# Performance work log

Measured on AMD Instinct MI355X. Metric: run time of the kernel, lower is better.

The kernel has to match this reference:

```python
import jax, jax.numpy as jnp
import numpy as np

EPS = 1e-06


def _conv1x1(x, W, b):
    # x: [B,C,H,W], W: [O,C], b: [O] -> [B,O,H,W]
    return jnp.einsum('oc,bchw->bohw', W, x) + b[None, :, None, None]


def _l2_norm(x):
    # normalize over channel dim (-2) per position, matching torch.norm(p=2, dim=-2)
    return x / jnp.linalg.norm(x, axis=-2, keepdims=True)


def setup_inputs() -> dict:
    key = jax.random.key(0)
    ks = jax.random.split(key, 8)
    B, C, H, W = 8, 512, 64, 64
    Cq = C // 8
    s = 0.02
    return {
        'x': jax.random.normal(ks[0], (B, C, H, W), jnp.float32),
        'Wq': jax.random.normal(ks[1], (Cq, C), jnp.float32) * s,
        'bq': jax.random.normal(ks[2], (Cq,), jnp.float32) * s,
        'Wk': jax.random.normal(ks[3], (Cq, C), jnp.float32) * s,
        'bk': jax.random.normal(ks[4], (Cq,), jnp.float32) * s,
        'Wv': jax.random.normal(ks[5], (C, C), jnp.float32) * s,
        'bv': jax.random.normal(ks[6], (C,), jnp.float32) * s,
        'gamma': jax.random.normal(ks[7], (1,), jnp.float32),
    }


def reference(x, Wq, bq, Wk, bk, Wv, bv, gamma):
    B, C, H, W = x.shape
    N = H * W
    Q = _conv1x1(x, Wq, bq).reshape(B, -1, N)   # [B,C',N]
    K = _conv1x1(x, Wk, bk).reshape(B, -1, N)   # [B,C',N]
    V = _conv1x1(x, Wv, bv).reshape(B, C, N)    # [B,C,N]

    Qn = _l2_norm(Q).transpose(0, 2, 1)         # [B,N,C']
    Kn = _l2_norm(K)                            # [B,C',N]

    # taylor denominator: 1 / (N + Q . (sum_n K + eps))
    tailor_sum = 1.0 / (N + jnp.einsum('bnc,bc->bn', Qn, Kn.sum(-1) + EPS))  # [B,N]

    value_sum = V.sum(-1)                        # [B,C]
    matrix = jnp.einsum('bmn,bcn->bmc', Kn, V)   # [B,C',C]
    matrix_sum = value_sum[:, :, None] + jnp.einsum('bnm,bmc->bcn', Qn, matrix)  # [B,C,N]

    weight_value = (matrix_sum * tailor_sum[:, None, :]).reshape(B, C, H, W)
    return gamma * weight_value
```

## Files before the change

### kernel.cpp

```cpp
#include <hip/hip_runtime.h>
#include <math.h>

#define B_   8
#define C_   512
#define CQ   64
#define N_   4096
#define EPSF 1e-6f
#define LS   40
#define LS2  72
#define LSF  552

typedef short  shortx8 __attribute__((ext_vector_type(8)));
typedef short  shortx4 __attribute__((ext_vector_type(4)));
typedef short  shortx2 __attribute__((ext_vector_type(2)));
typedef float  floatx4 __attribute__((ext_vector_type(4)));
typedef float  floatx2 __attribute__((ext_vector_type(2)));

__device__ __forceinline__ short f2bf(float f) {
    unsigned u = __builtin_bit_cast(unsigned, f);
    u += 0x7FFFu + ((u >> 16) & 1u);
    return (short)(u >> 16);
}
__device__ __forceinline__ float bf2f(short h) {
    unsigned u = ((unsigned)(unsigned short)h) << 16;
    return __builtin_bit_cast(float, u);
}
__device__ __forceinline__ shortx8 ldf8(const short* p) {
    return *(const shortx8*)p;
}

__global__ __launch_bounds__(256) void pcast(
    const float* __restrict__ Wq, const float* __restrict__ Wk,
    const float* __restrict__ Wv, short* __restrict__ Wqk, short* __restrict__ Wvb)
{
    int i = (blockIdx.x * 256 + threadIdx.x) * 4;
    float4 v; short* dst;
    if (i < 2 * CQ * C_) {
        const float* src = (i < CQ * C_) ? (Wq + i) : (Wk + i - CQ * C_);
        v = *(const float4*)src;
        dst = Wqk + i;
    } else {
        int j = i - 2 * CQ * C_;
        v = *(const float4*)(Wv + j);
        dst = Wvb + j;
    }
    const float* f = (const float*)&v;
    shortx4 o = { f2bf(f[0]), f2bf(f[1]), f2bf(f[2]), f2bf(f[3]) };
    *(shortx4*)dst = o;
}

__global__ __launch_bounds__(256, 2) void k1_qk(
    const float* __restrict__ x, const short* __restrict__ Wqk,
    const float* __restrict__ bq, const float* __restrict__ bk,
    short* __restrict__ Qnt, short* __restrict__ Kn, float* __restrict__ Ksum)
{
    const int b   = blockIdx.y;
    const int n0  = blockIdx.x * 64;
    const int tid = threadIdx.x;
    const int lane = tid & 63, wid = tid >> 6;
    const int waveM = wid >> 1, waveN = wid & 1;
    const int quad = lane >> 4, ln = lane & 15;

    __shared__ __attribute__((aligned(16))) short B_l[64][LSF];
    __shared__ float bias_l[128];

    if (tid < 128) bias_l[tid] = (tid < 64) ? bq[tid] : bk[tid - 64];

    const int nq = tid & 15, kp = tid >> 4;
    const float* xb = x + (size_t)b * C_ * N_;
#pragma unroll 4
    for (int i = 0; i < 16; i++) {
        const int k = kp * 2 + 32 * i;
        const float* p = xb + (size_t)k * N_ + n0 + nq * 4;
        float4 r0 = *(const float4*)(p);
        float4 r1 = *(const float4*)(p + N_);
        const float* f0 = (const float*)&r0;
        const float* f1 = (const float*)&r1;
#pragma unroll
        for (int j = 0; j < 4; j++) {
            shortx2 t = { f2bf(f0[j]), f2bf(f1[j]) };
            *(shortx2*)&B_l[nq * 4 + j][k] = t;
        }
    }
    __syncthreads();

    const short* Ab = Wqk + (size_t)(waveM * 64 + ln) * C_ + quad * 8;
    const floatx4 z4 = {0.f, 0.f, 0.f, 0.f};
    floatx4 acc[4][2];
#pragma unroll
    for (int mt = 0; mt < 4; mt++) { acc[mt][0] = z4; acc[mt][1] = z4; }

#pragma unroll 4
    for (int kc = 0; kc < 16; ++kc) {
        shortx8 af[4];
#pragma unroll
        for (int mt = 0; mt < 4; mt++)
            af[mt] = ldf8(Ab + (size_t)mt * 16 * C_ + kc * 32);
#pragma unroll
        for (int nt = 0; nt < 2; nt++) {
            shortx8 bf8 = ldf8(&B_l[waveN * 32 + nt * 16 + ln][kc * 32 + quad * 8]);
#pragma unroll
            for (int mt = 0; mt < 4; mt++)
                acc[mt][nt] = __builtin_amdgcn_mfma_f32_16x16x32_bf16(af[mt], bf8, acc[mt][nt], 0, 0, 0);
        }
    }

#pragma unroll
    for (int mt = 0; mt < 4; mt++)
#pragma unroll
        for (int r = 0; r < 4; r++) {
            float bias = bias_l[waveM * 64 + mt * 16 + quad * 4 + r];
#pragma unroll
            for (int nt = 0; nt < 2; nt++) acc[mt][nt][r] += bias;
        }
#pragma unroll
    for (int nt = 0; nt < 2; nt++) {
        float s = 0.f;
#pragma unroll
        for (int mt = 0; mt < 4; mt++)
#pragma unroll
            for (int r = 0; r < 4; r++) s += acc[mt][nt][r] * acc[mt][nt][r];
        s += __shfl_xor(s, 16);
        s += __shfl_xor(s, 32);
        float inv = rsqrtf(s);
#pragma unroll
        for (int mt = 0; mt < 4; mt++)
#pragma unroll
            for (int r = 0; r < 4; r++) acc[mt][nt][r] *= inv;
    }

    if (waveM == 0) {
        short* Qb = Qnt + (size_t)b * N_ * CQ;
#pragma unroll
        for (int nt = 0; nt < 2; nt++) {
            int n = n0 + waveN * 32 + nt * 16 + ln;
#pragma unroll
            for (int mt = 0; mt < 4; mt++) {
                shortx4 v;
#pragma unroll
                for (int r = 0; r < 4; r++) v[r] = f2bf(acc[mt][nt][r]);
                *(shortx4*)(Qb + (size_t)n * CQ + mt * 16 + quad * 4) = v;
            }
        }
    } else {
        short* Kb = Kn + (size_t)b * CQ * N_;
#pragma unroll
        for (int mt = 0; mt < 4; mt++)
#pragma unroll
            for (int r = 0; r < 4; r++) {
                int m = mt * 16 + quad * 4 + r;
                float s = 0.f;
#pragma unroll
                for (int nt = 0; nt < 2; nt++) {
                    int n = n0 + waveN * 32 + nt * 16 + ln;
                    float v = acc[mt][nt][r];
                    Kb[(size_t)m * N_ + n] = f2bf(v);
                    s += v;
                }
                s += __shfl_xor(s, 1); s += __shfl_xor(s, 2);
                s += __shfl_xor(s, 4); s += __shfl_xor(s, 8);
                if (ln == 0) atomicAdd(&Ksum[b * CQ + m], s);
            }
    }
}

__global__ __launch_bounds__(256, 2) void k2_kx(
    const float* __restrict__ x, const short* __restrict__ Kn,
    float* __restrict__ KX, float* __restrict__ xsum)
{
    const int jt = blockIdx.x, ks = blockIdx.y, b = blockIdx.z;
    const int j0 = jt * 64, nbase = ks * 512;
    const int tid = threadIdx.x;
    const int lane = tid & 63, wid = tid >> 6;
    const int quad = lane >> 4, ln = lane & 15;

    __shared__ __attribute__((aligned(16))) short B_l[64][LSF];

    const int rA = tid >> 2, oA = (tid & 3) * 8;
    const float* xb = x + (size_t)b * C_ * N_;
    const float* Bs = xb + (size_t)(j0 + rA) * N_ + nbase;

    float xsacc = 0.f;
#pragma unroll 4
    for (int i = 0; i < 16; i++) {
        const int n = oA + 32 * i;
        float4 b0 = *(const float4*)(Bs + n);
        float4 b1 = *(const float4*)(Bs + n + 4);
        const float* f0 = (const float*)&b0;
        const float* f1 = (const float*)&b1;
        shortx8 t;
#pragma unroll
        for (int q = 0; q < 4; q++) {
            t[q]     = f2bf(f0[q]); xsacc += f0[q];
            t[q + 4] = f2bf(f1[q]); xsacc += f1[q];
        }
        *(shortx8*)&B_l[rA][n] = t;
    }
    __syncthreads();

    const short* Kb = Kn + (size_t)b * CQ * N_;
    const short* Ab = Kb + (size_t)ln * N_ + nbase + quad * 8;
    const floatx4 z4 = {0.f, 0.f, 0.f, 0.f};
    floatx4 acc[4] = {z4, z4, z4, z4};

#pragma unroll 4
    for (int kc = 0; kc < 16; ++kc) {
        shortx8 af[4];
#pragma unroll
        for (int mt = 0; mt < 4; mt++)
            af[mt] = ldf8(Ab + (size_t)mt * 16 * N_ + kc * 32);
        shortx8 bf8 = ldf8(&B_l[wid * 16 + ln][kc * 32 + quad * 8]);
#pragma unroll
        for (int mt = 0; mt < 4; mt++)
            acc[mt] = __builtin_amdgcn_mfma_f32_16x16x32_bf16(af[mt], bf8, acc[mt], 0, 0, 0);
    }

    xsacc += __shfl_xor(xsacc, 1);
    xsacc += __shfl_xor(xsacc, 2);
    if ((tid & 3) == 0) atomicAdd(&xsum[b * C_ + j0 + rA], xsacc);

    float* KXb = KX + (size_t)b * CQ * C_;
#pragma unroll
    for (int mt = 0; mt < 4; mt++)
#pragma unroll
        for (int r = 0; r < 4; r++) {
            int m = mt * 16 + quad * 4 + r;
            atomicAdd(&KXb[(size_t)m * C_ + j0 + wid * 16 + ln], acc[mt][r]);
        }
}

__global__ __launch_bounds__(256, 2) void k3_m(
    const float* __restrict__ KX, const short* __restrict__ Wvb,
    const float* __restrict__ bv, const float* __restrict__ Ksum,
    const float* __restrict__ xsum,
    short* __restrict__ Mt, float* __restrict__ vs)
{
    const int ct = blockIdx.x, b = blockIdx.y;
    const int c0 = ct * 64;
    const int tid = threadIdx.x;
    const int lane = tid & 63, wid = tid >> 6;
    const int quad = lane >> 4, ln = lane & 15;

    __shared__ short A_l[2][64][LS];
    __shared__ short B_l[2][64][LS];
    __shared__ float xsl[C_], Ksl[64], bvl[64], vsp[4][64];

    xsl[tid] = xsum[(size_t)b * C_ + tid];
    xsl[tid + 256] = xsum[(size_t)b * C_ + tid + 256];
    if (tid < 64) { Ksl[tid] = Ksum[b * CQ + tid]; bvl[tid] = bv[c0 + tid]; }

    const int rA = tid >> 2, oA = (tid & 3) * 8;
    const short* As = Wvb + (size_t)(c0 + rA) * C_ + oA;
    const float* Bs = KX + ((size_t)b * CQ + rA) * C_ + oA;

    shortx8 aC = *(const shortx8*)As;
    float4 b0 = *(const float4*)(Bs);
    float4 b1 = *(const float4*)(Bs + 4);

    auto stage = [&](int buf, shortx8 a, float4 q0, float4 q1) {
        *(shortx8*)&A_l[buf][rA][oA] = a;
        const float* f0 = (const float*)&q0;
        const float* f1 = (const float*)&q1;
        shortx8 t;
#pragma unroll
        for (int i = 0; i < 4; i++) { t[i] = f2bf(f0[i]); t[i + 4] = f2bf(f1[i]); }
        *(shortx8*)&B_l[buf][rA][oA] = t;
    };
    stage(0, aC, b0, b1);
    __syncthreads();

    const floatx4 z4 = {0.f, 0.f, 0.f, 0.f};
    floatx4 acc[4] = {z4, z4, z4, z4};
    float vsacc = 0.f;
    const int cv = tid & 63;

    int cur = 0;
    for (int it = 0; it < 16; ++it) {
        shortx8 aN; float4 n0v, n1v;
        if (it < 15) {
            const int off = (it + 1) * 32;
            aN  = *(const shortx8*)(As + off);
            n0v = *(const float4*)(Bs + off);
            n1v = *(const float4*)(Bs + off + 4);
        }
        shortx8 af[4];
#pragma unroll
        for (int ct2 = 0; ct2 < 4; ct2++)
            af[ct2] = ldf8(&A_l[cur][ct2 * 16 + ln][quad * 8]);
        shortx8 bf8 = ldf8(&B_l[cur][wid * 16 + ln][quad * 8]);
#pragma unroll
        for (int ct2 = 0; ct2 < 4; ct2++)
            acc[ct2] = __builtin_amdgcn_mfma_f32_16x16x32_bf16(af[ct2], bf8, acc[ct2], 0, 0, 0);
#pragma unroll
        for (int jj = 0; jj < 8; jj++)
            vsacc += bf2f(A_l[cur][cv][wid * 8 + jj]) * xsl[it * 32 + wid * 8 + jj];
        if (it < 15) stage(cur ^ 1, aN, n0v, n1v);
        __syncthreads();
        cur ^= 1;
    }

    vsp[wid][cv] = vsacc;
    __syncthreads();
    if (tid < 64)
        vs[(size_t)b * C_ + c0 + tid] =
            vsp[0][tid] + vsp[1][tid] + vsp[2][tid] + vsp[3][tid] + (float)N_ * bvl[tid];

    const int m = wid * 16 + ln;
    const float ksm = Ksl[m];
    short* Mb = Mt + (size_t)b * C_ * CQ;
#pragma unroll
    for (int ct2 = 0; ct2 < 4; ct2++)
#pragma unroll
        for (int r = 0; r < 4; r++) {
            int c = ct2 * 16 + quad * 4 + r;
            Mb[(size_t)(c0 + c) * CQ + m] = f2bf(acc[ct2][r] + ksm * bvl[c]);
        }
}

__global__ __launch_bounds__(256, 3) void k4_out(
    const short* __restrict__ Qnt, const short* __restrict__ Mt,
    const float* __restrict__ vs, const float* __restrict__ Ksum,
    const float* __restrict__ gamma, float* __restrict__ out)
{
    const int nt = blockIdx.x, ct = blockIdx.y, b = blockIdx.z;
    const int n0 = nt * 128, c0 = ct * 128;
    const int tid = threadIdx.x;
    const int lane = tid & 63, wid = tid >> 6;
    const int waveC = wid >> 1, waveN = wid & 1;
    const int quad = lane >> 4, ln = lane & 15;

    __shared__ short A_l[128][LS2];
    __shared__ short B_l[128][LS2];
    __shared__ float tsl[128], vsl[128], Ks_l[64];

    {
        int c = tid >> 1, h = tid & 1;
        const short* src = Mt + ((size_t)b * C_ + c0 + c) * CQ + h * 32;
#pragma unroll
        for (int q = 0; q < 4; q++)
            *(shortx8*)&A_l[c][h * 32 + q * 8] = *(const shortx8*)(src + q * 8);
    }
    {
        int n = tid >> 1, h = tid & 1;
        const short* src = Qnt + ((size_t)b * N_ + n0 + n) * CQ + h * 32;
#pragma unroll
        for (int q = 0; q < 4; q++)
            *(shortx8*)&B_l[n][h * 32 + q * 8] = *(const shortx8*)(src + q * 8);
    }
    if (tid < 64)  Ks_l[tid] = Ksum[b * CQ + tid];
    if (tid < 128) vsl[tid]  = vs[(size_t)b * C_ + c0 + tid];
    __syncthreads();

    if (tid < 128) {
        const short* row = B_l[tid];
        float s = 0.f;
#pragma unroll
        for (int m = 0; m < 64; m++) s += bf2f(row[m]) * (Ks_l[m] + EPSF);
        tsl[tid] = 1.f / ((float)N_ + s);
    }
    __syncthreads();

    const floatx4 z4 = {0.f, 0.f, 0.f, 0.f};
    floatx4 acc[4][4];
#pragma unroll
    for (int i = 0; i < 4; i++)
#pragma unroll
        for (int j = 0; j < 4; j++) acc[i][j] = z4;

#pragma unroll
    for (int kc = 0; kc < 2; kc++) {
        shortx8 af[4];
#pragma unroll
        for (int ct2 = 0; ct2 < 4; ct2++)
            af[ct2] = ldf8(&A_l[waveC * 64 + ct2 * 16 + ln][kc * 32 + quad * 8]);
#pragma unroll
        for (int nt2 = 0; nt2 < 4; nt2++) {
            shortx8 bf8 = ldf8(&B_l[waveN * 64 + nt2 * 16 + ln][kc * 32 + quad * 8]);
#pragma unroll
            for (int ct2 = 0; ct2 < 4; ct2++)
                acc[ct2][nt2] = __builtin_amdgcn_mfma_f32_16x16x32_bf16(af[ct2], bf8, acc[ct2][nt2], 0, 0, 0);
        }
    }

    const float g = gamma[0];
    float* ob = out + (size_t)b * C_ * N_;
#pragma unroll
    for (int ct2 = 0; ct2 < 4; ct2++)
#pragma unroll
        for (int r = 0; r < 4; r++) {
            int cl = waveC * 64 + ct2 * 16 + quad * 4 + r;
            float vc = vsl[cl];
#pragma unroll
            for (int nt2 = 0; nt2 < 4; nt2++) {
                int nl = waveN * 64 + nt2 * 16 + ln;
                ob[(size_t)(c0 + cl) * N_ + n0 + nl] = g * tsl[nl] * (vc + acc[ct2][nt2][r]);
            }
        }
}

extern "C" void kernel_launch(void* const* d_in, const int* in_sizes, int n_in,
                              void* d_out, int out_size, void* d_ws, size_t ws_size,
                              hipStream_t stream)
{
    (void)in_sizes; (void)n_in; (void)out_size; (void)ws_size;
    const float* x     = (const float*)d_in[0];
    const float* Wq    = (const float*)d_in[1];
    const float* bq    = (const float*)d_in[2];
    const float* Wk    = (const float*)d_in[3];
    const float* bk    = (const float*)d_in[4];
    const float* Wv    = (const float*)d_in[5];
    const float* bv    = (const float*)d_in[6];
    const float* gamma = (const float*)d_in[7];
    float* out = (float*)d_out;

    short* Qnt = (short*)d_ws;
    short* Kn  = Qnt + (size_t)B_ * N_ * CQ;
    float* Ksum = (float*)(Kn + (size_t)B_ * CQ * N_);
    float* xsum = Ksum + B_ * CQ;
    float* KX   = xsum + B_ * C_;
    short* Mt   = (short*)(KX + (size_t)B_ * CQ * C_);
    float* vs   = (float*)(Mt + (size_t)B_ * C_ * CQ);
    short* Wqk  = (short*)(vs + B_ * C_);
    short* Wvb  = Wqk + 2 * CQ * C_;

    size_t zbytes = (size_t)(B_ * CQ + B_ * C_ + B_ * CQ * C_) * 4;
    hipMemsetAsync(Ksum, 0, zbytes, stream);

    pcast <<<dim3(320),      256, 0, stream>>>(Wq, Wk, Wv, Wqk, Wvb);
    k1_qk <<<dim3(64, 8),    256, 0, stream>>>(x, Wqk, bq, bk, Qnt, Kn, Ksum);
    k2_kx <<<dim3(8, 8, 8),  256, 0, stream>>>(x, Kn, KX, xsum);
    k3_m  <<<dim3(8, 8),     256, 0, stream>>>(KX, Wvb, bv, Ksum, xsum, Mt, vs);
    k4_out<<<dim3(32, 4, 8), 256, 0, stream>>>(Qnt, Mt, vs, Ksum, gamma, out);
}
```

Measured before the change: 198.8 us.

## Pre-transpose x to bf16 and stream operands directly from global memory

Adds an xprep kernel that casts x to bf16 and transposes it to an [N,C] layout, so k1 loads contiguous bf16 rows instead of doing a strided fp32 transpose-convert into shared memory. k2 drops its shared-memory staging, converts x fragments to bf16 in registers inside the MFMA loop, and raises occupancy to 4 blocks. k4 reads its Mt operand directly from global memory instead of staging it in LDS. This adds an extra pass over x (fp32 read plus bf16 write) and an extra launch, in exchange for cheaper loads in k1 and less LDS use in k2 and k4.

```diff
diff --git a/kernel.cpp b/kernel.cpp
--- a/kernel.cpp
+++ b/kernel.cpp
@@ -8,13 +8,12 @@
 #define EPSF 1e-6f
 #define LS   40
 #define LS2  72
-#define LSF  552
+#define LSX  520
+#define LTS  264
 
 typedef short  shortx8 __attribute__((ext_vector_type(8)));
 typedef short  shortx4 __attribute__((ext_vector_type(4)));
-typedef short  shortx2 __attribute__((ext_vector_type(2)));
 typedef float  floatx4 __attribute__((ext_vector_type(4)));
-typedef float  floatx2 __attribute__((ext_vector_type(2)));
 
 __device__ __forceinline__ short f2bf(float f) {
     unsigned u = __builtin_bit_cast(unsigned, f);
@@ -49,8 +48,35 @@
     *(shortx4*)dst = o;
 }
 
+__global__ __launch_bounds__(256, 2) void xprep(
+    const float* __restrict__ x, short* __restrict__ xT)
+{
+    const int cht = blockIdx.x, nt2 = blockIdx.y, b = blockIdx.z;
+    const int ch0 = cht * 256, n0 = nt2 * 128;
+    const int tid = threadIdx.x;
+
+    __shared__ __attribute__((aligned(16))) short T_l[128][LTS];
+
+    const float* src = x + ((size_t)b * C_ + ch0 + tid) * N_ + n0;
+#pragma unroll 8
+    for (int i = 0; i < 32; i++) {
+        float4 v = *(const float4*)(src + i * 4);
+        const float* f = (const float*)&v;
+#pragma unroll
+        for (int j = 0; j < 4; j++)
+            T_l[i * 4 + j][tid] = f2bf(f[j]);
+    }
+    __syncthreads();
+
+    const int n = tid >> 1, h = tid & 1;
+    short* dst = xT + ((size_t)b * N_ + n0 + n) * C_ + ch0 + h * 128;
+#pragma unroll
+    for (int i = 0; i < 16; i++)
+        *(shortx8*)(dst + i * 8) = *(const shortx8*)&T_l[n][h * 128 + i * 8];
+}
+
 __global__ __launch_bounds__(256, 2) void k1_qk(
-    const float* __restrict__ x, const short* __restrict__ Wqk,
+    const short* __restrict__ xT, const short* __restrict__ Wqk,
     const float* __restrict__ bq, const float* __restrict__ bk,
     short* __restrict__ Qnt, short* __restrict__ Kn, float* __restrict__ Ksum)
 {
@@ -61,26 +87,17 @@
     const int waveM = wid >> 1, waveN = wid & 1;
     const int quad = lane >> 4, ln = lane & 15;
 
-    __shared__ __attribute__((aligned(16))) short B_l[64][LSF];
+    __shared__ __attribute__((aligned(16))) short x_l[64][LSX];
     __shared__ float bias_l[128];
 
     if (tid < 128) bias_l[tid] = (tid < 64) ? bq[tid] : bk[tid - 64];
 
-    const int nq = tid & 15, kp = tid >> 4;
-    const float* xb = x + (size_t)b * C_ * N_;
-#pragma unroll 4
-    for (int i = 0; i < 16; i++) {
-        const int k = kp * 2 + 32 * i;
-        const float* p = xb + (size_t)k * N_ + n0 + nq * 4;
-        float4 r0 = *(const float4*)(p);
-        float4 r1 = *(const float4*)(p + N_);
-        const float* f0 = (const float*)&r0;
-        const float* f1 = (const float*)&r1;
-#pragma unroll
-        for (int j = 0; j < 4; j++) {
-            shortx2 t = { f2bf(f0[j]), f2bf(f1[j]) };
-            *(shortx2*)&B_l[nq * 4 + j][k] = t;
-        }
+    {
+        const int r = tid >> 2, off = (tid & 3) * 128;
+        const short* srcT = xT + ((size_t)b * N_ + n0 + r) * C_ + off;
+#pragma unroll
+        for (int i = 0; i < 16; i++)
+            *(shortx8*)&x_l[r][off + i * 8] = *(const shortx8*)(srcT + i * 8);
     }
     __syncthreads();
 
@@ -98,7 +115,7 @@
             af[mt] = ldf8(Ab + (size_t)mt * 16 * C_ + kc * 32);
 #pragma unroll
         for (int nt = 0; nt < 2; nt++) {
-            shortx8 bf8 = ldf8(&B_l[waveN * 32 + nt * 16 + ln][kc * 32 + quad * 8]);
+            shortx8 bf8 = ldf8(&x_l[waveN * 32 + nt * 16 + ln][kc * 32 + quad * 8]);
 #pragma unroll
             for (int mt = 0; mt < 4; mt++)
                 acc[mt][nt] = __builtin_amdgcn_mfma_f32_16x16x32_bf16(af[mt], bf8, acc[mt][nt], 0, 0, 0);
@@ -164,7 +181,7 @@
     }
 }
 
-__global__ __launch_bounds__(256, 2) void k2_kx(
+__global__ __launch_bounds__(256, 4) void k2_kx(
     const float* __restrict__ x, const short* __restrict__ Kn,
     float* __restrict__ KX, float* __restrict__ xsum)
 {
@@ -174,50 +191,38 @@
     const int lane = tid & 63, wid = tid >> 6;
     const int quad = lane >> 4, ln = lane & 15;
 
-    __shared__ __attribute__((aligned(16))) short B_l[64][LSF];
-
-    const int rA = tid >> 2, oA = (tid & 3) * 8;
-    const float* xb = x + (size_t)b * C_ * N_;
-    const float* Bs = xb + (size_t)(j0 + rA) * N_ + nbase;
-
-    float xsacc = 0.f;
-#pragma unroll 4
-    for (int i = 0; i < 16; i++) {
-        const int n = oA + 32 * i;
-        float4 b0 = *(const float4*)(Bs + n);
-        float4 b1 = *(const float4*)(Bs + n + 4);
-        const float* f0 = (const float*)&b0;
-        const float* f1 = (const float*)&b1;
-        shortx8 t;
-#pragma unroll
-        for (int q = 0; q < 4; q++) {
-            t[q]     = f2bf(f0[q]); xsacc += f0[q];
-            t[q + 4] = f2bf(f1[q]); xsacc += f1[q];
-        }
-        *(shortx8*)&B_l[rA][n] = t;
-    }
-    __syncthreads();
-
-    const short* Kb = Kn + (size_t)b * CQ * N_;
-    const short* Ab = Kb + (size_t)ln * N_ + nbase + quad * 8;
+    const short* Ab = Kn + (size_t)b * CQ * N_ + (size_t)ln * N_ + nbase + quad * 8;
+    const float* Bs = x + (size_t)b * C_ * N_
+                    + (size_t)(j0 + wid * 16 + ln) * N_ + nbase + quad * 8;
+
     const floatx4 z4 = {0.f, 0.f, 0.f, 0.f};
     floatx4 acc[4] = {z4, z4, z4, z4};
+    float xsacc = 0.f;
 
 #pragma unroll 4
     for (int kc = 0; kc < 16; ++kc) {
+        float4 u0 = *(const float4*)(Bs + kc * 32);
+        float4 u1 = *(const float4*)(Bs + kc * 32 + 4);
         shortx8 af[4];
 #pragma unroll
         for (int mt = 0; mt < 4; mt++)
             af[mt] = ldf8(Ab + (size_t)mt * 16 * N_ + kc * 32);
-        shortx8 bf8 = ldf8(&B_l[wid * 16 + ln][kc * 32 + quad * 8]);
+        const float* f0 = (const float*)&u0;
+        const float* f1 = (const float*)&u1;
+        shortx8 bf8;
+#pragma unroll
+        for (int q = 0; q < 4; q++) {
+            bf8[q]     = f2bf(f0[q]); xsacc += f0[q];
+            bf8[q + 4] = f2bf(f1[q]); xsacc += f1[q];
+        }
 #pragma unroll
         for (int mt = 0; mt < 4; mt++)
             acc[mt] = __builtin_amdgcn_mfma_f32_16x16x32_bf16(af[mt], bf8, acc[mt], 0, 0, 0);
     }
 
-    xsacc += __shfl_xor(xsacc, 1);
-    xsacc += __shfl_xor(xsacc, 2);
-    if ((tid & 3) == 0) atomicAdd(&xsum[b * C_ + j0 + rA], xsacc);
+    xsacc += __shfl_xor(xsacc, 16);
+    xsacc += __shfl_xor(xsacc, 32);
+    if (quad == 0) atomicAdd(&xsum[b * C_ + j0 + wid * 16 + ln], xsacc);
 
     float* KXb = KX + (size_t)b * CQ * C_;
 #pragma unroll
@@ -329,17 +334,9 @@
     const int waveC = wid >> 1, waveN = wid & 1;
     const int quad = lane >> 4, ln = lane & 15;
 
-    __shared__ short A_l[128][LS2];
     __shared__ short B_l[128][LS2];
     __shared__ float tsl[128], vsl[128], Ks_l[64];
 
-    {
-        int c = tid >> 1, h = tid & 1;
-        const short* src = Mt + ((size_t)b * C_ + c0 + c) * CQ + h * 32;
-#pragma unroll
-        for (int q = 0; q < 4; q++)
-            *(shortx8*)&A_l[c][h * 32 + q * 8] = *(const shortx8*)(src + q * 8);
-    }
     {
         int n = tid >> 1, h = tid & 1;
         const short* src = Qnt + ((size_t)b * N_ + n0 + n) * CQ + h * 32;
@@ -367,12 +364,14 @@
 #pragma unroll
         for (int j = 0; j < 4; j++) acc[i][j] = z4;
 
+    const short* Am = Mt + (size_t)b * C_ * CQ
+                    + (size_t)(c0 + waveC * 64 + ln) * CQ + quad * 8;
 #pragma unroll
     for (int kc = 0; kc < 2; kc++) {
         shortx8 af[4];
 #pragma unroll
         for (int ct2 = 0; ct2 < 4; ct2++)
-            af[ct2] = ldf8(&A_l[waveC * 64 + ct2 * 16 + ln][kc * 32 + quad * 8]);
+            af[ct2] = ldf8(Am + (size_t)ct2 * 16 * CQ + kc * 32);
 #pragma unroll
         for (int nt2 = 0; nt2 < 4; nt2++) {
             shortx8 bf8 = ldf8(&B_l[waveN * 64 + nt2 * 16 + ln][kc * 32 + quad * 8]);
@@ -422,13 +421,15 @@
     float* vs   = (float*)(Mt + (size_t)B_ * C_ * CQ);
     short* Wqk  = (short*)(vs + B_ * C_);
     short* Wvb  = Wqk + 2 * CQ * C_;
+    short* xT   = Wvb + (size_t)C_ * C_;
 
     size_t zbytes = (size_t)(B_ * CQ + B_ * C_ + B_ * CQ * C_) * 4;
     hipMemsetAsync(Ksum, 0, zbytes, stream);
 
-    pcast <<<dim3(320),      256, 0, stream>>>(Wq, Wk, Wv, Wqk, Wvb);
-    k1_qk <<<dim3(64, 8),    256, 0, stream>>>(x, Wqk, bq, bk, Qnt, Kn, Ksum);
-    k2_kx <<<dim3(8, 8, 8),  256, 0, stream>>>(x, Kn, KX, xsum);
-    k3_m  <<<dim3(8, 8),     256, 0, stream>>>(KX, Wvb, bv, Ksum, xsum, Mt, vs);
-    k4_out<<<dim3(32, 4, 8), 256, 0, stream>>>(Qnt, Mt, vs, Ksum, gamma, out);
-}
+    pcast <<<dim3(320),       256, 0, stream>>>(Wq, Wk, Wv, Wqk, Wvb);
+    xprep <<<dim3(2, 32, 8),  256, 0, stream>>>(x, xT);
+    k1_qk <<<dim3(64, 8),     256, 0, stream>>>(xT, Wqk, bq, bk, Qnt, Kn, Ksum);
+    k2_kx <<<dim3(8, 8, 8),   256, 0, stream>>>(x, Kn, KX, xsum);
+    k3_m  <<<dim3(8, 8),      256, 0, stream>>>(KX, Wvb, bv, Ksum, xsum, Mt, vs);
+    k4_out<<<dim3(32, 4, 8),  256, 0, stream>>>(Qnt, Mt, vs, Ksum, gamma, out);
+}
```

New measurement: 226.4 us. 1.14x slower.
